# Kernel tuning notes

Hardware: AMD Instinct MI355X
Metric: run time of the kernel (lower is better)

The kernel has to match this reference:

```python
import jax, jax.numpy as jnp
import numpy as np

D_MODEL = 1024
NUM_HEADS = 16
D_HEAD = 64
D_MLP = 4096
SEQ = 2048
BATCH = 4
NEG_BIG = 1e10


def setup_inputs() -> dict:
    key = jax.random.key(0)
    ks = jax.random.split(key, 10)
    s = 1.0 / np.sqrt(D_MODEL)
    return {
        "x": jax.random.normal(ks[0], (BATCH, SEQ, D_MODEL), dtype=jnp.float32),
        "W_K": jax.random.normal(ks[1], (NUM_HEADS, D_HEAD, D_MODEL), dtype=jnp.float32) * s,
        "W_Q": jax.random.normal(ks[2], (NUM_HEADS, D_HEAD, D_MODEL), dtype=jnp.float32) * s,
        "W_V": jax.random.normal(ks[3], (NUM_HEADS, D_HEAD, D_MODEL), dtype=jnp.float32) * s,
        "W_O": jax.random.normal(ks[4], (D_MODEL, D_HEAD * NUM_HEADS), dtype=jnp.float32) * s,
        "W_in": jax.random.normal(ks[5], (D_MLP, D_MODEL), dtype=jnp.float32) * s,
        "b_in": jnp.zeros((D_MLP,), dtype=jnp.float32),
        "W_out": jax.random.normal(ks[6], (D_MODEL, D_MLP), dtype=jnp.float32) * s,
        "b_out": jnp.zeros((D_MODEL,), dtype=jnp.float32),
    }


def _block(x, W_K, W_Q, W_V, W_O, W_in, b_in, W_out, b_out):
    seq = x.shape[1]
    # Attention
    k = jnp.einsum("ihd,bpd->biph", W_K, x)
    q = jnp.einsum("ihd,bpd->biph", W_Q, x)
    v = jnp.einsum("ihd,bpd->biph", W_V, x)
    scores = jnp.einsum("biph,biqh->biqp", k, q)  # [b, i, q(query), p(key)]
    mask = jnp.tril(jnp.ones((seq, seq), dtype=x.dtype))  # causal: key p <= query q
    scores = scores * mask - NEG_BIG * (1.0 - mask)
    attn = jax.nn.softmax(scores / np.sqrt(D_HEAD), axis=-1)
    z = jnp.einsum("biph,biqp->biqh", v, attn)  # [b, heads, q, d_head]
    z_flat = jnp.transpose(z, (0, 2, 1, 3)).reshape(z.shape[0], seq, -1)  # b q (i h)
    attn_out = jnp.einsum("df,bqf->bqd", W_O, z_flat)
    x = x + attn_out
    # MLP
    h = jnp.einsum("md,bpd->bpm", W_in, x) + b_in
    h = jax.nn.gelu(h, approximate=False)
    mlp_out = jnp.einsum("dm,bpm->bpd", W_out, h) + b_out
    return x + mlp_out


def reference(x, W_K, W_Q, W_V, W_O, W_in, b_in, W_out, b_out):
    return _block(x, W_K, W_Q, W_V, W_O, W_in, b_in, W_out, b_out)
```

## Files before the change

kernel.cpp:

```cpp
#include <hip/hip_runtime.h>
#include <hip/hip_bf16.h>

typedef __bf16 bf16;
typedef __bf16 bf16x8 __attribute__((ext_vector_type(8)));
typedef __bf16 bf16x4 __attribute__((ext_vector_type(4)));
typedef float  f32x4  __attribute__((ext_vector_type(4)));

#define MFMA(a,b,c) __builtin_amdgcn_mfma_f32_16x16x32_bf16(a,b,c,0,0,0)
#define EXP2F(x) __builtin_amdgcn_exp2f(x)

__device__ __forceinline__ void gload16(const void* g, void* l) {
  __builtin_amdgcn_global_load_lds((__attribute__((address_space(1))) void*)(g),
                                   (__attribute__((address_space(3))) void*)(l), 16, 0, 0);
}

struct CastSegs {
  const float* src[7];
  bf16* dst[7];
  int cum[8];
};

__global__ void cast_multi(CastSegs s) {
  int i = blockIdx.x * 256 + threadIdx.x;
  if (i >= s.cum[7]) return;
  int k = 0;
  #pragma unroll
  for (int j = 1; j < 7; ++j) if (i >= s.cum[j]) k = j;
  int off = i - s.cum[k];
  const float4* p = (const float4*)s.src[k];
  float4 a = p[2*off], b = p[2*off+1];
  bf16x8 v;
  v[0]=(bf16)a.x; v[1]=(bf16)a.y; v[2]=(bf16)a.z; v[3]=(bf16)a.w;
  v[4]=(bf16)b.x; v[5]=(bf16)b.y; v[6]=(bf16)b.z; v[7]=(bf16)b.w;
  *(bf16x8*)(s.dst[k] + (size_t)8*off) = v;
}

__device__ __forceinline__ float gelu_t(float s) {
  float u = s * (0.7978845608f + 0.0356774081f * s * s);
  return s / (1.0f + EXP2F(-2.885390082f * u));
}

#define LGKM0_FENCE() { asm volatile("s_waitcnt lgkmcnt(0)" ::: "memory"); \
                        __builtin_amdgcn_sched_barrier(0); }


#define LDA_PH(MI2) { _Pragma("unroll") for (int i = 0; i < 4; i++) { \
    af[i][0] = *(const bf16x8*)(lds + ab + ((((MI2)<<2)+i) << 11) + rdswz); \
    af[i][1] = *(const bf16x8*)(lds + ab + ((((MI2)<<2)+i) << 11) + 1024 + rdswz); } }

#define LDB_PH(NI2) { _Pragma("unroll") for (int n = 0; n < 2; n++) { \
    bfr[((NI2)<<1)+n][0] = *(const bf16x8*)(lds + bb + (((((NI2)<<1)+n)) << 11) + rdswz); \
    bfr[((NI2)<<1)+n][1] = *(const bf16x8*)(lds + bb + (((((NI2)<<1)+n)) << 11) + 1024 + rdswz); } }

#define MM_PH(MI2, NI2) { __builtin_amdgcn_s_setprio(1); \
    _Pragma("unroll") for (int i = 0; i < 4; i++) \
      _Pragma("unroll") for (int n = 0; n < 2; n++) { \
        acc[((MI2)<<2)+i][((NI2)<<1)+n] = MFMA(af[i][0], bfr[((NI2)<<1)+n][0], acc[((MI2)<<2)+i][((NI2)<<1)+n]); \
        acc[((MI2)<<2)+i][((NI2)<<1)+n] = MFMA(af[i][1], bfr[((NI2)<<1)+n][1], acc[((MI2)<<2)+i][((NI2)<<1)+n]); } \
    __builtin_amdgcn_s_setprio(0); }

#define GTILE(CUR, S1, S2, VM) { \
    const int ab = ((CUR) << 16) + (wm << 14); \
    const int bb = ((CUR) << 16) + 32768 + (wn << 13); \
    LDA_PH(0); LDB_PH(0); \
    if (S1) STG(sA, (CUR)^1, 0, 1, t + 1); \
    asm volatile("s_waitcnt lgkmcnt(8)" ::: "memory"); \
    __builtin_amdgcn_s_barrier(); LGKM0_FENCE(); \
    MM_PH(0, 0); \
    LDB_PH(1); \
    if (S2) STG(sB, (CUR), 1, 0, t + 2); \
    __builtin_amdgcn_s_barrier(); LGKM0_FENCE(); \
    MM_PH(0, 1); \
    LDA_PH(1); \
    if (S2) STG(sB, (CUR), 1, 1, t + 2); \
    __builtin_amdgcn_s_barrier(); LGKM0_FENCE(); \
    MM_PH(1, 0); \
    if (S2) STG(sA, (CUR), 0, 0, t + 2); \
    MM_PH(1, 1); \
    asm volatile("s_waitcnt vmcnt(" #VM ")" ::: "memory"); \
    __builtin_amdgcn_s_barrier(); \
    __builtin_amdgcn_sched_barrier(0); }

template<int EPI>
__global__ __launch_bounds__(512, 2) void gemm256(
    const bf16* __restrict__ A, const bf16* __restrict__ B,
    float* __restrict__ outf, bf16* __restrict__ outb,
    const bf16* __restrict__ addb, const float* __restrict__ bias,
    bf16* __restrict__ vtb,
    int M, int N, int K, int gx)
{
  __shared__ __attribute__((aligned(128))) char lds[131072];
  const int tid = threadIdx.x;
  const int w = tid >> 6, l = tid & 63, lg = l >> 4, li = l & 15;
  const int wm = w >> 2, wn = w & 3;

  const int nwg = gridDim.x, orig = blockIdx.x;
  const int q = nwg >> 3, r = nwg & 7;
  const int xcd = orig & 7, pos = orig >> 3;
  const int wg = (xcd < r ? xcd*(q+1) : r*(q+1) + (xcd-r)*q) + pos;
  const int m0 = (wg / gx) << 8, n0 = (wg % gx) << 8;

  const int NT = K >> 6;

  const int srow = ((tid >> 7) << 4) + ((tid >> 2) & 15);
  const int scol = (((tid >> 6) & 1) << 5) + (((tid & 3) << 3) ^ (((tid >> 5) & 1) << 4));
  const bf16* sA = A + (size_t)(m0 + srow) * K + scol;
  const bf16* sB = B + (size_t)(n0 + srow) * K + scol;
  char* const myl = lds + (w << 10);

  auto STG = [&](const bf16* s0, int buf, int isB, int h, int tt) {
    const bf16* g = s0 + ((size_t)(h << 7)) * K + ((size_t)tt << 6);
    char* lb = myl + (buf << 16) + (isB << 15) + (h << 14);
    gload16(g, lb);
    gload16(g + ((size_t)K << 6), lb + 8192);
  };

  const int rdswz = (li << 6) + ((lg << 4) ^ ((li & 8) << 2));

  f32x4 acc[8][4] = {};
  bf16x8 af[4][2], bfr[4][2];

  STG(sB, 0, 1, 0, 0); STG(sB, 0, 1, 1, 0); STG(sA, 0, 0, 0, 0); STG(sA, 0, 0, 1, 0);
  asm volatile("s_waitcnt vmcnt(4)" ::: "memory");
  STG(sB, 1, 1, 0, 1); STG(sB, 1, 1, 1, 1); STG(sA, 1, 0, 0, 1);
  asm volatile("s_waitcnt vmcnt(6)" ::: "memory");
  __builtin_amdgcn_s_barrier();
  __builtin_amdgcn_sched_barrier(0);

  int t = 0;
  for (int tt = 0; tt + 3 < NT; tt += 2) {
    t = tt;     GTILE(0, 1, 1, 6);
    t = tt + 1; GTILE(1, 1, 1, 6);
  }
  t = NT - 2; GTILE(0, 1, 0, 0);
  t = NT - 1; GTILE(1, 0, 0, 0);

  if (EPI == 0 && n0 >= 2048) {
    #pragma unroll
    for (int mi = 0; mi < 8; mi++) {
      const int row = m0 + (wm << 7) + (mi << 4) + (lg << 2);
      const int p = row & 2047;
      const size_t bhb = (size_t)((row >> 11) << 4);
      #pragma unroll
      for (int ni = 0; ni < 4; ni++) {
        const int col = n0 + (wn << 6) + (ni << 4) + li;
        const int hh = (col >> 6) & 15, dd = col & 63;
        bf16x4 pk;
        pk[0] = (bf16)acc[mi][ni][0]; pk[1] = (bf16)acc[mi][ni][1];
        pk[2] = (bf16)acc[mi][ni][2]; pk[3] = (bf16)acc[mi][ni][3];
        *(bf16x4*)(vtb + ((bhb + hh) * 64 + dd) * 2048 + p) = pk;
      }
    }
    return;
  }

  #pragma unroll
  for (int mi = 0; mi < 8; mi++) {
    const int row = m0 + (wm << 7) + (mi << 4) + (lg << 2);
    #pragma unroll
    for (int ni = 0; ni < 4; ni++) {
      const int col = n0 + (wn << 6) + (ni << 4) + li;
      #pragma unroll
      for (int r2 = 0; r2 < 4; r2++) {
        const size_t idx = (size_t)(row + r2) * N + col;
        float v = acc[mi][ni][r2];
        if (EPI == 0) {
          outb[idx] = (bf16)v;
        } else if (EPI == 1) {
          outb[idx] = (bf16)(v + (float)addb[idx]);
        } else if (EPI == 2) {
          outb[idx] = (bf16)gelu_t(v + bias[col]);
        } else {
          outf[idx] = v + bias[col] + (float)addb[idx];
        }
      }
    }
  }
}

#define N_LDA2(BMI) { _Pragma("unroll") for (int i = 0; i < 2; i++) { \
    af[i][0] = *(const bf16x8*)(lds + abase + (((BMI)+i) << 11) + rdswz); \
    af[i][1] = *(const bf16x8*)(lds + abase + (((BMI)+i) << 11) + 1024 + rdswz); } }

#define N_LDB2(BNI) { _Pragma("unroll") for (int n = 0; n < 2; n++) { \
    bfr[(BNI)+n][0] = *(const bf16x8*)(lds + bbase + (((BNI)+n) << 11) + rdswz); \
    bfr[(BNI)+n][1] = *(const bf16x8*)(lds + bbase + (((BNI)+n) << 11) + 1024 + rdswz); } }

#define N_MMQ(MB, NB) { __builtin_amdgcn_s_setprio(1); \
    _Pragma("unroll") for (int i = 0; i < 2; i++) \
      _Pragma("unroll") for (int n = 0; n < 2; n++) { \
        acc[((MB)<<1)+i][((NB)<<1)+n] = MFMA(af[i][0], bfr[((NB)<<1)+n][0], acc[((MB)<<1)+i][((NB)<<1)+n]); \
        acc[((MB)<<1)+i][((NB)<<1)+n] = MFMA(af[i][1], bfr[((NB)<<1)+n][1], acc[((MB)<<1)+i][((NB)<<1)+n]); } \
    __builtin_amdgcn_s_setprio(0); }

#define NTILE(CUR, S1, S2, VM) { \
    const int abase = (CUR) * 49152 + ((wm >> 1) << 14) + ((wm & 1) << 13); \
    const int bbase = (CUR) * 49152 + 32768 + (wn << 13); \
    N_LDA2(0); N_LDB2(0); \
    if (S1) STA((CUR)^1, 1, t + 1); \
    __builtin_amdgcn_s_barrier(); LGKM0_FENCE(); \
    N_MMQ(0, 0); \
    N_LDB2(2); \
    if (S2) STB((CUR), 0, t + 2); \
    __builtin_amdgcn_s_barrier(); LGKM0_FENCE(); \
    N_MMQ(0, 1); \
    N_LDA2(2); \
    if (S2) STB((CUR), 1, t + 2); \
    __builtin_amdgcn_s_barrier(); LGKM0_FENCE(); \
    N_MMQ(1, 0); \
    if (S2) STA((CUR), 0, t + 2); \
    N_MMQ(1, 1); \
    asm volatile("s_waitcnt vmcnt(" #VM ")" ::: "memory"); \
    __builtin_amdgcn_s_barrier(); \
    __builtin_amdgcn_sched_barrier(0); }

template<int EPI>
__global__ __launch_bounds__(512, 2) void gemm128n(
    const bf16* __restrict__ A, const bf16* __restrict__ B,
    float* __restrict__ outf, bf16* __restrict__ outb,
    const bf16* __restrict__ addb, const float* __restrict__ bias,
    bf16* __restrict__ vtb,
    int M, int N, int K, int gx)
{
  __shared__ __attribute__((aligned(128))) char lds[98304];
  const int tid = threadIdx.x;
  const int w = tid >> 6, l = tid & 63, lg = l >> 4, li = l & 15;
  const int wm = w >> 1, wn = w & 1;

  const int nwg = gridDim.x, orig = blockIdx.x;
  const int q = nwg >> 3, r = nwg & 7;
  const int xcd = orig & 7, pos = orig >> 3;
  const int wg = (xcd < r ? xcd*(q+1) : r*(q+1) + (xcd-r)*q) + pos;
  const int m0 = (wg / gx) << 8, n0 = (wg % gx) << 7;

  const int NT = K >> 6;

  const int srow = ((tid >> 7) << 4) + ((tid >> 2) & 15);
  const int scol = (((tid >> 6) & 1) << 5) + (((tid & 3) << 3) ^ (((tid >> 5) & 1) << 4));
  const bf16* sA = A + (size_t)(m0 + srow) * K + scol;
  const bf16* sB = B + (size_t)(n0 + srow) * K + scol;
  char* const myl = lds + (w << 10);

  auto STA = [&](int buf, int h, int tt) {
    const bf16* g = sA + ((size_t)(h << 7)) * K + ((size_t)tt << 6);
    char* lb = myl + buf * 49152 + (h << 14);
    gload16(g, lb);
    gload16(g + ((size_t)K << 6), lb + 8192);
  };
  auto STB = [&](int buf, int h, int tt) {
    const bf16* g = sB + ((size_t)(h << 6)) * K + ((size_t)tt << 6);
    gload16(g, myl + buf * 49152 + 32768 + (h << 13));
  };

  const int rdswz = (li << 6) + ((lg << 4) ^ ((li & 8) << 2));

  f32x4 acc[4][4] = {};
  bf16x8 af[2][2], bfr[4][2];

  STB(0, 0, 0); STB(0, 1, 0); STA(0, 0, 0); STA(0, 1, 0);
  STB(1, 0, 1); STB(1, 1, 1); STA(1, 0, 1);
  asm volatile("s_waitcnt vmcnt(4)" ::: "memory");
  __builtin_amdgcn_s_barrier();
  __builtin_amdgcn_sched_barrier(0);

  int t = 0;
  for (int tt = 0; tt + 3 < NT; tt += 2) {
    t = tt;     NTILE(0, 1, 1, 4);
    t = tt + 1; NTILE(1, 1, 1, 4);
  }
  t = NT - 2; NTILE(0, 1, 0, 0);
  t = NT - 1; NTILE(1, 0, 0, 0);

  if (EPI == 0 && n0 >= 2048) {
    #pragma unroll
    for (int mi = 0; mi < 4; mi++) {
      const int row = m0 + (wm << 6) + (mi << 4) + (lg << 2);
      const int p = row & 2047;
      const size_t bhb = (size_t)((row >> 11) << 4);
      #pragma unroll
      for (int ni = 0; ni < 4; ni++) {
        const int col = n0 + (wn << 6) + (ni << 4) + li;
        const int hh = (col >> 6) & 15, dd = col & 63;
        bf16x4 pk;
        pk[0] = (bf16)acc[mi][ni][0]; pk[1] = (bf16)acc[mi][ni][1];
        pk[2] = (bf16)acc[mi][ni][2]; pk[3] = (bf16)acc[mi][ni][3];
        *(bf16x4*)(vtb + ((bhb + hh) * 64 + dd) * 2048 + p) = pk;
      }
    }
    return;
  }

  #pragma unroll
  for (int mi = 0; mi < 4; mi++) {
    const int row = m0 + (wm << 6) + (mi << 4) + (lg << 2);
    #pragma unroll
    for (int ni = 0; ni < 4; ni++) {
      const int col = n0 + (wn << 6) + (ni << 4) + li;
      #pragma unroll
      for (int r2 = 0; r2 < 4; r2++) {
        const size_t idx = (size_t)(row + r2) * N + col;
        float v = acc[mi][ni][r2];
        if (EPI == 0) {
          outb[idx] = (bf16)v;
        } else if (EPI == 1) {
          outb[idx] = (bf16)(v + (float)addb[idx]);
        } else if (EPI == 2) {
          outb[idx] = (bf16)gelu_t(v + bias[col]);
        } else {
          outf[idx] = v + bias[col] + (float)addb[idx];
        }
      }
    }
  }
}

__global__ __launch_bounds__(256) void attn_kernel(const bf16* __restrict__ qkv,
                                                   const bf16* __restrict__ vt,
                                                   bf16* __restrict__ z)
{
  __shared__ bf16 Ksh[2][64*64];
  __shared__ bf16 Vsh[2][64*64];
  __shared__ bf16 Pl[4*16*64];

  const int tid = threadIdx.x;
  const int w = tid >> 6, l = tid & 63, lg = l >> 4, li = l & 15;
  const int orig = blockIdx.x;
  const int xcd = orig & 7, sub = orig >> 3;
  const int bh = (xcd << 3) + (sub >> 4);
  const int pr = sub & 15;
  const int h = bh & 15, b = bh >> 4;
  const size_t tb = (size_t)b * 2048;

  const int srow = tid >> 3, sc = tid & 7;
  const bf16* Kg = qkv + (tb + srow) * 3072 + 1024 + (h << 6) + ((sc ^ (srow & 7)) << 3);
  const bf16* Vg = vt + ((size_t)bh * 64 + srow) * 2048 + ((sc ^ (srow & 7)) << 3);

  char* pw = (char*)Pl + (w << 11) + li * 128;
  const int psw = (li & 3) << 5;

  for (int hf = 0; hf < 2; ++hf) {
    const int qt = hf ? pr : (31 - pr);
    const int qw = (qt << 6) + (w << 4);

    const bf16* Qp = qkv + (tb + qw + li) * 3072 + (h << 6);
    bf16x8 qa0 = *(const bf16x8*)(Qp + (lg << 3));
    bf16x8 qa1 = *(const bf16x8*)(Qp + 32 + (lg << 3));
    #pragma unroll
    for (int e = 0; e < 8; e++) {
      qa0[e] = (bf16)((float)qa0[e] * 0.1803368801f);
      qa1[e] = (bf16)((float)qa1[e] * 0.1803368801f);
    }

    f32x4 zacc[4] = {};
    float mR = -1e30f, lS = 0.f;
    const int nkt = qt + 1;

    gload16(Kg,                   (bf16*)Ksh[0] + (w << 9));
    gload16(Kg + (size_t)32*3072, (bf16*)Ksh[0] + 2048 + (w << 9));
    gload16(Vg,                   (bf16*)Vsh[0] + (w << 9));
    gload16(Vg + (size_t)32*2048, (bf16*)Vsh[0] + 2048 + (w << 9));
    __syncthreads();

    for (int kt = 0; kt < nkt; ++kt) {
      const int cur = kt & 1;
      const int pb = kt << 6;

      if (kt + 1 < nkt) {
        const int nb = cur ^ 1;
        const size_t ko = (size_t)(pb + 64) * 3072;
        gload16(Kg + ko,                   (bf16*)Ksh[nb] + (w << 9));
        gload16(Kg + ko + (size_t)32*3072, (bf16*)Ksh[nb] + 2048 + (w << 9));
        gload16(Vg + pb + 64,                   (bf16*)Vsh[nb] + (w << 9));
        gload16(Vg + pb + 64 + (size_t)32*2048, (bf16*)Vsh[nb] + 2048 + (w << 9));
      }

      f32x4 s[4];
      __builtin_amdgcn_s_setprio(1);
      #pragma unroll
      for (int sub2 = 0; sub2 < 4; ++sub2) {
        const char* kr = (const char*)Ksh[cur] + ((sub2 << 4) + li) * 128;
        const int c0 = (lg ^ (li & 7)) << 4;
        bf16x8 kb0 = *(const bf16x8*)(kr + c0);
        bf16x8 kb1 = *(const bf16x8*)(kr + (c0 ^ 64));
        f32x4 a2 = {};
        a2 = MFMA(kb0, qa0, a2);
        a2 = MFMA(kb1, qa1, a2);
        s[sub2] = a2;
      }
      __builtin_amdgcn_s_setprio(0);

      if (pb + 63 > qw) {
        #pragma unroll
        for (int sub2 = 0; sub2 < 4; ++sub2)
          #pragma unroll
          for (int r = 0; r < 4; ++r)
            if (pb + (sub2 << 4) + (lg << 2) + r > qw + li) s[sub2][r] = -1e30f;
      }

      f32x4 m4;
      #pragma unroll
      for (int r = 0; r < 4; ++r)
        m4[r] = fmaxf(fmaxf(s[0][r], s[1][r]), fmaxf(s[2][r], s[3][r]));
      float lmx = fmaxf(fmaxf(m4[0], m4[1]), fmaxf(m4[2], m4[3]));

      float mn = mR;
      if (!__all(lmx <= mR + 11.5f)) {
        float mx = fmaxf(lmx, __shfl_xor(lmx, 16));
        mx = fmaxf(mx, __shfl_xor(mx, 32));
        mn = fmaxf(mR, mx);
        float c = EXP2F(mR - mn);
        mR = mn;
        lS *= c;
        float cr0 = __shfl(c, (lg << 2) + 0);
        float cr1 = __shfl(c, (lg << 2) + 1);
        float cr2 = __shfl(c, (lg << 2) + 2);
        float cr3 = __shfl(c, (lg << 2) + 3);
        #pragma unroll
        for (int d = 0; d < 4; ++d) {
          zacc[d][0] *= cr0; zacc[d][1] *= cr1;
          zacc[d][2] *= cr2; zacc[d][3] *= cr3;
        }
      }

      f32x4 p[4];
      #pragma unroll
      for (int sub2 = 0; sub2 < 4; ++sub2)
        #pragma unroll
        for (int r = 0; r < 4; ++r)
          p[sub2][r] = EXP2F(s[sub2][r] - mn);
      f32x4 t4 = p[0] + p[1] + p[2] + p[3];
      lS += (t4[0] + t4[1]) + (t4[2] + t4[3]);

      #pragma unroll
      for (int sub2 = 0; sub2 < 4; ++sub2) {
        bf16x4 pk;
        pk[0] = (bf16)p[sub2][0]; pk[1] = (bf16)p[sub2][1];
        pk[2] = (bf16)p[sub2][2]; pk[3] = (bf16)p[sub2][3];
        *(bf16x4*)(pw + (((sub2 << 5) + (lg << 3)) ^ psw)) = pk;
      }

      __builtin_amdgcn_s_setprio(1);
      #pragma unroll
      for (int kc = 0; kc < 2; ++kc) {
        bf16x8 pa = *(const bf16x8*)(pw + (((kc << 6) + (lg << 4)) ^ psw));
        #pragma unroll
        for (int d = 0; d < 4; ++d) {
          const char* vr = (const char*)Vsh[cur] + ((d << 4) + li) * 128;
          bf16x8 vb = *(const bf16x8*)(vr + ((((kc << 2) + lg) ^ (li & 7)) << 4));
          zacc[d] = MFMA(pa, vb, zacc[d]);
        }
      }
      __builtin_amdgcn_s_setprio(0);

      __syncthreads();
    }

    lS += __shfl_xor(lS, 16);
    lS += __shfl_xor(lS, 32);

    float rls[4];
    #pragma unroll
    for (int r = 0; r < 4; ++r) rls[r] = 1.0f / __shfl(lS, (lg << 2) + r);
    bf16* zp = z + (tb + qw) * 1024 + (h << 6);
    #pragma unroll
    for (int d = 0; d < 4; ++d)
      #pragma unroll
      for (int r = 0; r < 4; ++r)
        zp[(size_t)((lg << 2) + r) * 1024 + (d << 4) + li] = (bf16)(zacc[d][r] * rls[r]);
  }
}

extern "C" void kernel_launch(void* const* d_in, const int* in_sizes, int n_in,
                              void* d_out, int out_size, void* d_ws, size_t ws_size,
                              hipStream_t stream)
{
  const float* x     = (const float*)d_in[0];
  const float* W_K   = (const float*)d_in[1];
  const float* W_Q   = (const float*)d_in[2];
  const float* W_V   = (const float*)d_in[3];
  const float* W_O   = (const float*)d_in[4];
  const float* W_in  = (const float*)d_in[5];
  const float* b_in  = (const float*)d_in[6];
  const float* W_out = (const float*)d_in[7];
  const float* b_out = (const float*)d_in[8];
  float* out = (float*)d_out;

  char* ws = (char*)d_ws;
  bf16*  xb   = (bf16*)ws;  ws += (size_t)8192*1024*2;
  bf16*  wqkv = (bf16*)ws;  ws += (size_t)3072*1024*2;
  bf16*  wo   = (bf16*)ws;  ws += (size_t)1024*1024*2;
  bf16*  win  = (bf16*)ws;  ws += (size_t)4096*1024*2;
  bf16*  wout = (bf16*)ws;  ws += (size_t)1024*4096*2;
  bf16*  qkv  = (bf16*)ws;  ws += (size_t)8192*3072*2;
  bf16*  zb   = (bf16*)ws;  ws += (size_t)8192*1024*2;
  bf16*  x1b  = (bf16*)ws;  ws += (size_t)8192*1024*2;
  bf16*  hb   = (bf16*)ws;
  bf16*  vtb  = hb;

  CastSegs cs;
  const float* srcs[7] = { x, W_Q, W_K, W_V, W_O, W_in, W_out };
  bf16* dsts[7] = { xb, wqkv, wqkv + 1024*1024, wqkv + 2048*1024, wo, win, wout };
  int n8s[7] = { 1048576, 131072, 131072, 131072, 131072, 524288, 524288 };
  int cum = 0;
  for (int i = 0; i < 7; ++i) { cs.src[i] = srcs[i]; cs.dst[i] = dsts[i]; cs.cum[i] = cum; cum += n8s[i]; }
  cs.cum[7] = cum;
  cast_multi<<<dim3((cum + 255) / 256), dim3(256), 0, stream>>>(cs);

  gemm128n<0><<<dim3(768), 512, 0, stream>>>(xb, wqkv, nullptr, qkv, nullptr, nullptr, vtb, 8192, 3072, 1024, 24);
  attn_kernel<<<dim3(1024), 256, 0, stream>>>(qkv, vtb, zb);
  gemm128n<1><<<dim3(256), 512, 0, stream>>>(zb, wo, nullptr, x1b, xb, nullptr, nullptr, 8192, 1024, 1024, 8);
  gemm256<2><<<dim3(512), 512, 0, stream>>>(x1b, win, nullptr, hb, nullptr, b_in, nullptr, 8192, 4096, 1024, 16);
  gemm128n<3><<<dim3(256), 512, 0, stream>>>(hb, wout, out, nullptr, x1b, b_out, nullptr, 8192, 1024, 4096, 8);
}
```

Measured before the change: 296.7 us.

## Make GEMM kernels persistent and prefetch the next tile during the epilogue

Converts the GEMM kernels into persistent loops in which each of 256 workgroups processes several output tiles in sequence. The global-to-LDS loads for the next tile are issued before the current tile's epilogue stores, so the prologue overlaps the output writes. This aims to remove launch and wave-tail overhead and hide the pipeline fill. In exchange, a grid of exactly 256 workgroups may leave CUs idle or unbalanced, and the added vmcnt(0) wait plus barrier adds a sync point between tiles.

```diff
diff --git a/kernel.cpp b/kernel.cpp
--- a/kernel.cpp
+++ b/kernel.cpp
@@ -87,7 +87,7 @@
     float* __restrict__ outf, bf16* __restrict__ outb,
     const bf16* __restrict__ addb, const float* __restrict__ bias,
     bf16* __restrict__ vtb,
-    int M, int N, int K, int gx)
+    int M, int N, int K, int gx, int TILES)
 {
   __shared__ __attribute__((aligned(128))) char lds[131072];
   const int tid = threadIdx.x;
@@ -98,16 +98,14 @@
   const int q = nwg >> 3, r = nwg & 7;
   const int xcd = orig & 7, pos = orig >> 3;
   const int wg = (xcd < r ? xcd*(q+1) : r*(q+1) + (xcd-r)*q) + pos;
-  const int m0 = (wg / gx) << 8, n0 = (wg % gx) << 8;
 
   const int NT = K >> 6;
 
   const int srow = ((tid >> 7) << 4) + ((tid >> 2) & 15);
   const int scol = (((tid >> 6) & 1) << 5) + (((tid & 3) << 3) ^ (((tid >> 5) & 1) << 4));
-  const bf16* sA = A + (size_t)(m0 + srow) * K + scol;
-  const bf16* sB = B + (size_t)(n0 + srow) * K + scol;
   char* const myl = lds + (w << 10);
 
+  const bf16 *sA, *sB;
   auto STG = [&](const bf16* s0, int buf, int isB, int h, int tt) {
     const bf16* g = s0 + ((size_t)(h << 7)) * K + ((size_t)tt << 6);
     char* lb = myl + (buf << 16) + (isB << 15) + (h << 14);
@@ -117,8 +115,11 @@
 
   const int rdswz = (li << 6) + ((lg << 4) ^ ((li & 8) << 2));
 
-  f32x4 acc[8][4] = {};
   bf16x8 af[4][2], bfr[4][2];
+
+  int m0 = (wg / gx) << 8, n0 = (wg % gx) << 8;
+  sA = A + (size_t)(m0 + srow) * K + scol;
+  sB = B + (size_t)(n0 + srow) * K + scol;
 
   STG(sB, 0, 1, 0, 0); STG(sB, 0, 1, 1, 0); STG(sA, 0, 0, 0, 0); STG(sA, 0, 0, 1, 0);
   asm volatile("s_waitcnt vmcnt(4)" ::: "memory");
@@ -127,53 +128,72 @@
   __builtin_amdgcn_s_barrier();
   __builtin_amdgcn_sched_barrier(0);
 
-  int t = 0;
-  for (int tt = 0; tt + 3 < NT; tt += 2) {
-    t = tt;     GTILE(0, 1, 1, 6);
-    t = tt + 1; GTILE(1, 1, 1, 6);
-  }
-  t = NT - 2; GTILE(0, 1, 0, 0);
-  t = NT - 1; GTILE(1, 0, 0, 0);
-
-  if (EPI == 0 && n0 >= 2048) {
-    #pragma unroll
-    for (int mi = 0; mi < 8; mi++) {
-      const int row = m0 + (wm << 7) + (mi << 4) + (lg << 2);
-      const int p = row & 2047;
-      const size_t bhb = (size_t)((row >> 11) << 4);
-      #pragma unroll
-      for (int ni = 0; ni < 4; ni++) {
-        const int col = n0 + (wn << 6) + (ni << 4) + li;
-        const int hh = (col >> 6) & 15, dd = col & 63;
-        bf16x4 pk;
-        pk[0] = (bf16)acc[mi][ni][0]; pk[1] = (bf16)acc[mi][ni][1];
-        pk[2] = (bf16)acc[mi][ni][2]; pk[3] = (bf16)acc[mi][ni][3];
-        *(bf16x4*)(vtb + ((bhb + hh) * 64 + dd) * 2048 + p) = pk;
-      }
-    }
-    return;
-  }
-
-  #pragma unroll
-  for (int mi = 0; mi < 8; mi++) {
-    const int row = m0 + (wm << 7) + (mi << 4) + (lg << 2);
-    #pragma unroll
-    for (int ni = 0; ni < 4; ni++) {
-      const int col = n0 + (wn << 6) + (ni << 4) + li;
-      #pragma unroll
-      for (int r2 = 0; r2 < 4; r2++) {
-        const size_t idx = (size_t)(row + r2) * N + col;
-        float v = acc[mi][ni][r2];
-        if (EPI == 0) {
-          outb[idx] = (bf16)v;
-        } else if (EPI == 1) {
-          outb[idx] = (bf16)(v + (float)addb[idx]);
-        } else if (EPI == 2) {
-          outb[idx] = (bf16)gelu_t(v + bias[col]);
-        } else {
-          outf[idx] = v + bias[col] + (float)addb[idx];
+  for (int rt = 0; rt < TILES; ++rt) {
+    f32x4 acc[8][4] = {};
+
+    int t = 0;
+    for (int tt = 0; tt + 3 < NT; tt += 2) {
+      t = tt;     GTILE(0, 1, 1, 6);
+      t = tt + 1; GTILE(1, 1, 1, 6);
+    }
+    t = NT - 2; GTILE(0, 1, 0, 0);
+    t = NT - 1; GTILE(1, 0, 0, 0);
+
+    const int em0 = m0, en0 = n0;
+    if (rt + 1 < TILES) {
+      const int wt = wg + (rt + 1) * nwg;
+      m0 = (wt / gx) << 8; n0 = (wt % gx) << 8;
+      sA = A + (size_t)(m0 + srow) * K + scol;
+      sB = B + (size_t)(n0 + srow) * K + scol;
+      STG(sB, 0, 1, 0, 0); STG(sB, 0, 1, 1, 0); STG(sA, 0, 0, 0, 0); STG(sA, 0, 0, 1, 0);
+      STG(sB, 1, 1, 0, 1); STG(sB, 1, 1, 1, 1); STG(sA, 1, 0, 0, 1);
+    }
+
+    if (EPI == 0 && en0 >= 2048) {
+      #pragma unroll
+      for (int mi = 0; mi < 8; mi++) {
+        const int row = em0 + (wm << 7) + (mi << 4) + (lg << 2);
+        const int p = row & 2047;
+        const size_t bhb = (size_t)((row >> 11) << 4);
+        #pragma unroll
+        for (int ni = 0; ni < 4; ni++) {
+          const int col = en0 + (wn << 6) + (ni << 4) + li;
+          const int hh = (col >> 6) & 15, dd = col & 63;
+          bf16x4 pk;
+          pk[0] = (bf16)acc[mi][ni][0]; pk[1] = (bf16)acc[mi][ni][1];
+          pk[2] = (bf16)acc[mi][ni][2]; pk[3] = (bf16)acc[mi][ni][3];
+          *(bf16x4*)(vtb + ((bhb + hh) * 64 + dd) * 2048 + p) = pk;
         }
       }
+    } else {
+      #pragma unroll
+      for (int mi = 0; mi < 8; mi++) {
+        const int row = em0 + (wm << 7) + (mi << 4) + (lg << 2);
+        #pragma unroll
+        for (int ni = 0; ni < 4; ni++) {
+          const int col = en0 + (wn << 6) + (ni << 4) + li;
+          #pragma unroll
+          for (int r2 = 0; r2 < 4; r2++) {
+            const size_t idx = (size_t)(row + r2) * N + col;
+            float v = acc[mi][ni][r2];
+            if (EPI == 0) {
+              outb[idx] = (bf16)v;
+            } else if (EPI == 1) {
+              outb[idx] = (bf16)(v + (float)addb[idx]);
+            } else if (EPI == 2) {
+              outb[idx] = (bf16)gelu_t(v + bias[col]);
+            } else {
+              outf[idx] = v + bias[col] + (float)addb[idx];
+            }
+          }
+        }
+      }
+    }
+
+    if (rt + 1 < TILES) {
+      asm volatile("s_waitcnt vmcnt(0)" ::: "memory");
+      __builtin_amdgcn_s_barrier();
+      __builtin_amdgcn_sched_barrier(0);
     }
   }
 }
@@ -220,7 +240,7 @@
     float* __restrict__ outf, bf16* __restrict__ outb,
     const bf16* __restrict__ addb, const float* __restrict__ bias,
     bf16* __restrict__ vtb,
-    int M, int N, int K, int gx)
+    int M, int N, int K, int gx, int TILES)
 {
   __shared__ __attribute__((aligned(128))) char lds[98304];
   const int tid = threadIdx.x;
@@ -231,16 +251,14 @@
   const int q = nwg >> 3, r = nwg & 7;
   const int xcd = orig & 7, pos = orig >> 3;
   const int wg = (xcd < r ? xcd*(q+1) : r*(q+1) + (xcd-r)*q) + pos;
-  const int m0 = (wg / gx) << 8, n0 = (wg % gx) << 7;
 
   const int NT = K >> 6;
 
   const int srow = ((tid >> 7) << 4) + ((tid >> 2) & 15);
   const int scol = (((tid >> 6) & 1) << 5) + (((tid & 3) << 3) ^ (((tid >> 5) & 1) << 4));
-  const bf16* sA = A + (size_t)(m0 + srow) * K + scol;
-  const bf16* sB = B + (size_t)(n0 + srow) * K + scol;
   char* const myl = lds + (w << 10);
 
+  const bf16 *sA, *sB;
   auto STA = [&](int buf, int h, int tt) {
     const bf16* g = sA + ((size_t)(h << 7)) * K + ((size_t)tt << 6);
     char* lb = myl + buf * 49152 + (h << 14);
@@ -254,8 +272,11 @@
 
   const int rdswz = (li << 6) + ((lg << 4) ^ ((li & 8) << 2));
 
-  f32x4 acc[4][4] = {};
   bf16x8 af[2][2], bfr[4][2];
+
+  int m0 = (wg / gx) << 8, n0 = (wg % gx) << 7;
+  sA = A + (size_t)(m0 + srow) * K + scol;
+  sB = B + (size_t)(n0 + srow) * K + scol;
 
   STB(0, 0, 0); STB(0, 1, 0); STA(0, 0, 0); STA(0, 1, 0);
   STB(1, 0, 1); STB(1, 1, 1); STA(1, 0, 1);
@@ -263,53 +284,72 @@
   __builtin_amdgcn_s_barrier();
   __builtin_amdgcn_sched_barrier(0);
 
-  int t = 0;
-  for (int tt = 0; tt + 3 < NT; tt += 2) {
-    t = tt;     NTILE(0, 1, 1, 4);
-    t = tt + 1; NTILE(1, 1, 1, 4);
-  }
-  t = NT - 2; NTILE(0, 1, 0, 0);
-  t = NT - 1; NTILE(1, 0, 0, 0);
-
-  if (EPI == 0 && n0 >= 2048) {
-    #pragma unroll
-    for (int mi = 0; mi < 4; mi++) {
-      const int row = m0 + (wm << 6) + (mi << 4) + (lg << 2);
-      const int p = row & 2047;
-      const size_t bhb = (size_t)((row >> 11) << 4);
-      #pragma unroll
-      for (int ni = 0; ni < 4; ni++) {
-        const int col = n0 + (wn << 6) + (ni << 4) + li;
-        const int hh = (col >> 6) & 15, dd = col & 63;
-        bf16x4 pk;
-        pk[0] = (bf16)acc[mi][ni][0]; pk[1] = (bf16)acc[mi][ni][1];
-        pk[2] = (bf16)acc[mi][ni][2]; pk[3] = (bf16)acc[mi][ni][3];
-        *(bf16x4*)(vtb + ((bhb + hh) * 64 + dd) * 2048 + p) = pk;
-      }
-    }
-    return;
-  }
-
-  #pragma unroll
-  for (int mi = 0; mi < 4; mi++) {
-    const int row = m0 + (wm << 6) + (mi << 4) + (lg << 2);
-    #pragma unroll
-    for (int ni = 0; ni < 4; ni++) {
-      const int col = n0 + (wn << 6) + (ni << 4) + li;
-      #pragma unroll
-      for (int r2 = 0; r2 < 4; r2++) {
-        const size_t idx = (size_t)(row + r2) * N + col;
-        float v = acc[mi][ni][r2];
-        if (EPI == 0) {
-          outb[idx] = (bf16)v;
-        } else if (EPI == 1) {
-          outb[idx] = (bf16)(v + (float)addb[idx]);
-        } else if (EPI == 2) {
-          outb[idx] = (bf16)gelu_t(v + bias[col]);
-        } else {
-          outf[idx] = v + bias[col] + (float)addb[idx];
+  for (int rt = 0; rt < TILES; ++rt) {
+    f32x4 acc[4][4] = {};
+
+    int t = 0;
+    for (int tt = 0; tt + 3 < NT; tt += 2) {
+      t = tt;     NTILE(0, 1, 1, 4);
+      t = tt + 1; NTILE(1, 1, 1, 4);
+    }
+    t = NT - 2; NTILE(0, 1, 0, 0);
+    t = NT - 1; NTILE(1, 0, 0, 0);
+
+    const int em0 = m0, en0 = n0;
+    if (rt + 1 < TILES) {
+      const int wt = wg + (rt + 1) * nwg;
+      m0 = (wt / gx) << 8; n0 = (wt % gx) << 7;
+      sA = A + (size_t)(m0 + srow) * K + scol;
+      sB = B + (size_t)(n0 + srow) * K + scol;
+      STB(0, 0, 0); STB(0, 1, 0); STA(0, 0, 0); STA(0, 1, 0);
+      STB(1, 0, 1); STB(1, 1, 1); STA(1, 0, 1);
+    }
+
+    if (EPI == 0 && en0 >= 2048) {
+      #pragma unroll
+      for (int mi = 0; mi < 4; mi++) {
+        const int row = em0 + (wm << 6) + (mi << 4) + (lg << 2);
+        const int p = row & 2047;
+        const size_t bhb = (size_t)((row >> 11) << 4);
+        #pragma unroll
+        for (int ni = 0; ni < 4; ni++) {
+          const int col = en0 + (wn << 6) + (ni << 4) + li;
+          const int hh = (col >> 6) & 15, dd = col & 63;
+          bf16x4 pk;
+          pk[0] = (bf16)acc[mi][ni][0]; pk[1] = (bf16)acc[mi][ni][1];
+          pk[2] = (bf16)acc[mi][ni][2]; pk[3] = (bf16)acc[mi][ni][3];
+          *(bf16x4*)(vtb + ((bhb + hh) * 64 + dd) * 2048 + p) = pk;
         }
       }
+    } else {
+      #pragma unroll
+      for (int mi = 0; mi < 4; mi++) {
+        const int row = em0 + (wm << 6) + (mi << 4) + (lg << 2);
+        #pragma unroll
+        for (int ni = 0; ni < 4; ni++) {
+          const int col = en0 + (wn << 6) + (ni << 4) + li;
+          #pragma unroll
+          for (int r2 = 0; r2 < 4; r2++) {
+            const size_t idx = (size_t)(row + r2) * N + col;
+            float v = acc[mi][ni][r2];
+            if (EPI == 0) {
+              outb[idx] = (bf16)v;
+            } else if (EPI == 1) {
+              outb[idx] = (bf16)(v + (float)addb[idx]);
+            } else if (EPI == 2) {
+              outb[idx] = (bf16)gelu_t(v + bias[col]);
+            } else {
+              outf[idx] = v + bias[col] + (float)addb[idx];
+            }
+          }
+        }
+      }
+    }
+
+    if (rt + 1 < TILES) {
+      asm volatile("s_waitcnt vmcnt(0)" ::: "memory");
+      __builtin_amdgcn_s_barrier();
+      __builtin_amdgcn_sched_barrier(0);
     }
   }
 }
@@ -506,9 +546,9 @@
   cs.cum[7] = cum;
   cast_multi<<<dim3((cum + 255) / 256), dim3(256), 0, stream>>>(cs);
 
-  gemm128n<0><<<dim3(768), 512, 0, stream>>>(xb, wqkv, nullptr, qkv, nullptr, nullptr, vtb, 8192, 3072, 1024, 24);
+  gemm128n<0><<<dim3(256), 512, 0, stream>>>(xb, wqkv, nullptr, qkv, nullptr, nullptr, vtb, 8192, 3072, 1024, 24, 3);
   attn_kernel<<<dim3(1024), 256, 0, stream>>>(qkv, vtb, zb);
-  gemm128n<1><<<dim3(256), 512, 0, stream>>>(zb, wo, nullptr, x1b, xb, nullptr, nullptr, 8192, 1024, 1024, 8);
-  gemm256<2><<<dim3(512), 512, 0, stream>>>(x1b, win, nullptr, hb, nullptr, b_in, nullptr, 8192, 4096, 1024, 16);
-  gemm128n<3><<<dim3(256), 512, 0, stream>>>(hb, wout, out, nullptr, x1b, b_out, nullptr, 8192, 1024, 4096, 8);
-}
+  gemm128n<1><<<dim3(256), 512, 0, stream>>>(zb, wo, nullptr, x1b, xb, nullptr, nullptr, 8192, 1024, 1024, 8, 1);
+  gemm256<2><<<dim3(256), 512, 0, stream>>>(x1b, win, nullptr, hb, nullptr, b_in, nullptr, 8192, 4096, 1024, 16, 2);
+  gemm128n<3><<<dim3(256), 512, 0, stream>>>(hb, wout, out, nullptr, x1b, b_out, nullptr, 8192, 1024, 4096, 8, 1);
+}
```

Result: slower. 317.4 us (+7.0%).
